# Kernel tuning notes

Measured on AMD Instinct MI355X. Metric: run time of the kernel, lower is better.

## Reference

```python
import jax, jax.numpy as jnp
import numpy as np

NUM_HEADS = 8
LN_EPS = 1e-5


def _layernorm(x, g, b):
    mu = jnp.mean(x, axis=-1, keepdims=True)
    var = jnp.mean((x - mu) ** 2, axis=-1, keepdims=True)
    return (x - mu) * jax.lax.rsqrt(var + LN_EPS) * g + b


def setup_inputs() -> dict:
    key = jax.random.key(0)
    B, T, N, D = 16, 12, 325, 128
    F = 256
    ks = jax.random.split(key, 16)
    s = 0.02
    return {
        "x": jax.random.normal(ks[0], (B, T, N, D), dtype=jnp.float32),
        "Wq": jax.random.normal(ks[1], (D, D), dtype=jnp.float32) * s,
        "bq": jnp.zeros((D,), jnp.float32),
        "Wk": jax.random.normal(ks[2], (D, D), dtype=jnp.float32) * s,
        "bk": jnp.zeros((D,), jnp.float32),
        "Wv": jax.random.normal(ks[3], (D, D), dtype=jnp.float32) * s,
        "bv": jnp.zeros((D,), jnp.float32),
        "Wo": jax.random.normal(ks[4], (D, D), dtype=jnp.float32) * s,
        "bo": jnp.zeros((D,), jnp.float32),
        "ln1_g": jnp.ones((D,), jnp.float32),
        "ln1_b": jnp.zeros((D,), jnp.float32),
        "W1": jax.random.normal(ks[5], (D, F), dtype=jnp.float32) * s,
        "b1": jnp.zeros((F,), jnp.float32),
        "W2": jax.random.normal(ks[6], (F, D), dtype=jnp.float32) * s,
        "b2": jnp.zeros((D,), jnp.float32),
        "ln2_g": jnp.ones((D,), jnp.float32),
        "ln2_b": jnp.zeros((D,), jnp.float32),
    }


def reference(x, Wq, bq, Wk, bk, Wv, bv, Wo, bo, ln1_g, ln1_b, W1, b1, W2, b2, ln2_g, ln2_b):
    B, T, N, D = x.shape
    H = NUM_HEADS
    hd = D // H
    # Conv2d 1x1 projections == per-channel linear over last dim
    q = (x @ Wq + bq).reshape(B, T, N, H, hd)
    k = (x @ Wk + bk).reshape(B, T, N, H, hd)
    v = (x @ Wv + bv).reshape(B, T, N, H, hd)
    # attention across the node dim (n,m), per (batch, head, time)
    scores = jnp.einsum("btnhd,btmhd->bhtnm", q, k) / jnp.sqrt(jnp.float32(hd))
    attn = jax.nn.softmax(scores, axis=-1)
    out = jnp.einsum("bhtnm,btmhd->btnhd", attn, v).reshape(B, T, N, D)
    out = out @ Wo + bo
    out = _layernorm(x + out, ln1_g, ln1_b)
    ffn = jax.nn.gelu(out @ W1 + b1, approximate=False) @ W2 + b2
    return _layernorm(out + ffn, ln2_g, ln2_b)
```

## Files before the change

### kernel.cpp

```cpp
#include <hip/hip_runtime.h>
#include <hip/hip_bf16.h>
#include <math.h>

#define B_ 16
#define T_ 12
#define N_ 325
#define D_ 128
#define H_ 8
#define HD_ 16
#define F_ 256
#define ROWS (B_*T_*N_)
#define NP 336
#define QK_STRIDE 20
#define VT_STRIDE 340
#define LN_EPS 1e-5f

typedef __hip_bfloat16 bf16;
typedef __attribute__((ext_vector_type(8))) short bf16x8;
typedef __attribute__((ext_vector_type(4))) short bf16x4;
typedef __attribute__((ext_vector_type(4))) float f32x4;

__device__ __forceinline__ float b2f(bf16 v) { return __bfloat162float(v); }
__device__ __forceinline__ bf16  f2b(float v) { return __float2bfloat16(v); }

__device__ __forceinline__ float fexp2(float v) { return __builtin_amdgcn_exp2f(v); }
__device__ __forceinline__ float frcp(float v) { return __builtin_amdgcn_rcpf(v); }

union frag_cvt  { uint4 u; bf16x8 s; };
union frag4_cvt { uint2 u; bf16x4 s; };
union h2u       { __hip_bfloat162 h; unsigned u; };

__device__ __forceinline__ bf16x8 frag_ld(const void* p) {
    frag_cvt c; c.u = *(const uint4*)p; return c.s;
}
__device__ __forceinline__ bf16x4 frag4_ld(const void* p) {
    frag4_cvt c; c.u = *(const uint2*)p; return c.s;
}

__device__ __forceinline__ unsigned pk2(float a, float b) {
    h2u c; c.h = __float22bfloat162_rn(make_float2(a, b)); return c.u;
}

__device__ __forceinline__ bf16x4 pack4_rtn(f32x4 v) {
    frag4_cvt c;
    c.u.x = pk2(v[0], v[1]);
    c.u.y = pk2(v[2], v[3]);
    return c.s;
}

__device__ __forceinline__ bf16x8 pack8_rtn(float4 a, float4 b) {
    frag_cvt c;
    c.u.x = pk2(a.x, a.y);
    c.u.y = pk2(a.z, a.w);
    c.u.z = pk2(b.x, b.y);
    c.u.w = pk2(b.z, b.w);
    return c.s;
}

__device__ __forceinline__ float gelu_fast(float a) {
    float z = fexp2(2.3022083f * a * (1.f + 0.044715f * a * a));
    return a * z * frcp(z + 1.f);
}

#define MFMA16(a_, b_, c_) __builtin_amdgcn_mfma_f32_16x16x16bf16_1k((a_), (b_), (c_), 0, 0, 0)
#define MFMA32(a_, b_, c_) __builtin_amdgcn_mfma_f32_16x16x32_bf16((a_), (b_), (c_), 0, 0, 0)

__global__ void convert_weights(const float* __restrict__ Wq, const float* __restrict__ Wk,
                                const float* __restrict__ Wv, const float* __restrict__ Wo,
                                const float* __restrict__ W1, const float* __restrict__ W2,
                                bf16* __restrict__ wt) {
    int i = blockIdx.x * 256 + threadIdx.x;
    if (i < 16384)       { int k = i >> 7, n = i & 127;                    wt[n * 128 + k] = f2b(Wq[i]); }
    else if (i < 32768)  { int j = i - 16384; int k = j >> 7, n = j & 127; wt[16384 + n * 128 + k] = f2b(Wk[j]); }
    else if (i < 49152)  { int j = i - 32768; int k = j >> 7, n = j & 127; wt[32768 + n * 128 + k] = f2b(Wv[j]); }
    else if (i < 65536)  { int j = i - 49152; int k = j >> 7, n = j & 127;
                           wt[49152 + n * 128 + (k ^ ((n & 7) << 3))] = f2b(Wo[j]); }
    else if (i < 98304)  { int j = i - 65536; int k = j >> 8, n = j & 255;
                           wt[65536 + n * 128 + (k ^ ((n & 7) << 3))] = f2b(W1[j]); }
    else                 { int j = i - 98304; int k = j >> 7, n = j & 127;
                           wt[98304 + n * 256 + (k ^ ((n & 7) << 3))] = f2b(W2[j]); }
}

__global__ __launch_bounds__(256) void qkv_attn_kernel(
        const float* __restrict__ x, const bf16* __restrict__ wt,
        const float* __restrict__ bq, const float* __restrict__ bk,
        const float* __restrict__ bv, bf16* __restrict__ ao) {
    __shared__ __align__(16) bf16 qsh[NP * QK_STRIDE];
    __shared__ __align__(16) bf16 ksh[NP * QK_STRIDE];
    __shared__ __align__(16) bf16 vsh_t[HD_ * VT_STRIDE];

    int bid  = blockIdx.x;
    int bt   = bid % 192;
    int h    = bid / 192;
    int tid  = threadIdx.x;
    int wave = tid >> 6;
    int lane = tid & 63;
    int lm   = lane & 15;
    int quad = lane >> 4;

    bf16x8 bfrag[3][4];
    #pragma unroll
    for (int mat = 0; mat < 3; mat++) {
        const bf16* Wt = wt + mat * 16384 + (size_t)(h * 16 + lm) * 128;
        #pragma unroll
        for (int ks = 0; ks < 4; ks++)
            bfrag[mat][ks] = frag_ld(Wt + ks * 32 + quad * 8);
    }
    float bqv = bq[h * 16 + lm], bkv = bk[h * 16 + lm], bvv = bv[h * 16 + lm];
    const float QSCALE = 0.25f * 1.44269504f;

    const float* xslab = x + (size_t)bt * N_ * D_;
    for (int mt = wave; mt < 21; mt += 4) {
        int row  = mt * 16 + lm;
        int crow = row < N_ ? row : N_ - 1;
        const float* xr = xslab + (size_t)crow * D_;
        bf16x8 af[4];
        #pragma unroll
        for (int ks = 0; ks < 4; ks++) {
            const float4* p = (const float4*)(xr + ks * 32 + quad * 8);
            af[ks] = pack8_rtn(p[0], p[1]);
        }
        f32x4 cq = {0.f,0.f,0.f,0.f}, ck = {0.f,0.f,0.f,0.f}, cv = {0.f,0.f,0.f,0.f};
        #pragma unroll
        for (int ks = 0; ks < 4; ks++) {
            cq = MFMA32(af[ks], bfrag[0][ks], cq);
            ck = MFMA32(af[ks], bfrag[1][ks], ck);
            cv = MFMA32(af[ks], bfrag[2][ks], cv);
        }
        #pragma unroll
        for (int reg = 0; reg < 4; reg++) {
            int r = mt * 16 + quad * 4 + reg;
            bool v = r < N_;
            qsh[r * QK_STRIDE + lm]  = f2b(v ? (cq[reg] + bqv) * QSCALE : 0.f);
            ksh[r * QK_STRIDE + lm]  = f2b(v ? (ck[reg] + bkv) : 0.f);
            vsh_t[lm * VT_STRIDE + r] = f2b(v ? (cv[reg] + bvv) : 0.f);
        }
    }
    __syncthreads();

    const f32x4 zero = {0.f, 0.f, 0.f, 0.f};
    for (int qt0 = wave; qt0 < 21; qt0 += 8) {
        int qt1  = qt0 + 4;
        int qt1c = qt1 < 21 ? qt1 : 20;
        bf16x4 qf0 = frag4_ld(qsh + (qt0  * 16 + lm) * QK_STRIDE + quad * 4);
        bf16x4 qf1 = frag4_ld(qsh + (qt1c * 16 + lm) * QK_STRIDE + quad * 4);
        f32x4 o0 = zero, o1 = zero;
        float L0 = 0.f, L1 = 0.f;
        for (int kt = 0; kt < 20; kt++) {
            bf16x4 kf = frag4_ld(ksh + (kt * 16 + lm) * QK_STRIDE + quad * 4);
            bf16x4 vf = frag4_ld(vsh_t + lm * VT_STRIDE + kt * 16 + quad * 4);
            f32x4 s0 = MFMA16(kf, qf0, zero);
            f32x4 s1 = MFMA16(kf, qf1, zero);
            f32x4 p0, p1;
            p0[0] = fexp2(s0[0]); p0[1] = fexp2(s0[1]);
            p0[2] = fexp2(s0[2]); p0[3] = fexp2(s0[3]);
            p1[0] = fexp2(s1[0]); p1[1] = fexp2(s1[1]);
            p1[2] = fexp2(s1[2]); p1[3] = fexp2(s1[3]);
            L0 += (p0[0] + p0[1]) + (p0[2] + p0[3]);
            L1 += (p1[0] + p1[1]) + (p1[2] + p1[3]);
            o0 = MFMA16(vf, pack4_rtn(p0), o0);
            o1 = MFMA16(vf, pack4_rtn(p1), o1);
        }
        {
            bf16x4 kf = frag4_ld(ksh + (20 * 16 + lm) * QK_STRIDE + quad * 4);
            bf16x4 vf = frag4_ld(vsh_t + lm * VT_STRIDE + 20 * 16 + quad * 4);
            f32x4 s0 = MFMA16(kf, qf0, zero);
            f32x4 s1 = MFMA16(kf, qf1, zero);
            f32x4 p0, p1;
            #pragma unroll
            for (int reg = 0; reg < 4; reg++) {
                bool ok = (quad * 4 + reg) < 5;
                p0[reg] = ok ? fexp2(s0[reg]) : 0.f;
                p1[reg] = ok ? fexp2(s1[reg]) : 0.f;
            }
            L0 += (p0[0] + p0[1]) + (p0[2] + p0[3]);
            L1 += (p1[0] + p1[1]) + (p1[2] + p1[3]);
            o0 = MFMA16(vf, pack4_rtn(p0), o0);
            o1 = MFMA16(vf, pack4_rtn(p1), o1);
        }
        L0 += __shfl_xor(L0, 16, 64); L0 += __shfl_xor(L0, 32, 64);
        L1 += __shfl_xor(L1, 16, 64); L1 += __shfl_xor(L1, 32, 64);
        float i0 = frcp(L0), i1 = frcp(L1);
        int n0 = qt0 * 16 + lm;
        if (n0 < N_) {
            frag4_cvt o;
            o.u.x = pk2(o0[0] * i0, o0[1] * i0);
            o.u.y = pk2(o0[2] * i0, o0[3] * i0);
            *(uint2*)(ao + ((size_t)bt * N_ + n0) * D_ + h * HD_ + quad * 4) = o.u;
        }
        int n1 = qt1 * 16 + lm;
        if (qt1 < 21 && n1 < N_) {
            frag4_cvt o;
            o.u.x = pk2(o1[0] * i1, o1[1] * i1);
            o.u.y = pk2(o1[2] * i1, o1[3] * i1);
            *(uint2*)(ao + ((size_t)bt * N_ + n1) * D_ + h * HD_ + quad * 4) = o.u;
        }
    }
}

#define US_STRIDE 136
#define H_STRIDE  264

__global__ __launch_bounds__(256) void epi_a(
        const float* __restrict__ x, const bf16* __restrict__ ao,
        const bf16* __restrict__ wt, const float* __restrict__ bo,
        const float* __restrict__ g1, const float* __restrict__ be1,
        bf16* __restrict__ usg) {
    __shared__ __align__(16) bf16 wbuf[16384];

    const bf16* Wot = wt + 49152;
    int tid  = threadIdx.x;
    int wave = tid >> 6;
    int lm   = tid & 15;
    int quad = (tid & 63) >> 4;
    int r0   = blockIdx.x * 64 + wave * 16;
    int sw   = (lm & 7) << 3;

    bf16x8 afrag[4];
    {
        const bf16* ar = ao + (size_t)(r0 + lm) * D_;
        #pragma unroll
        for (int ks = 0; ks < 4; ks++)
            afrag[ks] = frag_ld(ar + ks * 32 + quad * 8);
    }
    {
        const uint4* gs = (const uint4*)Wot;
        uint4*       ls = (uint4*)wbuf;
        #pragma unroll
        for (int i = 0; i < 8; i++) ls[tid + i * 256] = gs[tid + i * 256];
    }
    __syncthreads();

    f32x4 acc[8];
    #pragma unroll
    for (int nt = 0; nt < 8; nt++) {
        f32x4 c = {0.f, 0.f, 0.f, 0.f};
        const bf16* w = wbuf + (size_t)(nt * 16 + lm) * 128;
        #pragma unroll
        for (int ks = 0; ks < 4; ks++) {
            bf16x8 b = frag_ld(w + ((ks * 32 + quad * 8) ^ sw));
            c = MFMA32(afrag[ks], b, c);
        }
        acc[nt] = c;
    }

    float bov[8], g1v[8], be1v[8];
    #pragma unroll
    for (int nt = 0; nt < 8; nt++) {
        int col = nt * 16 + lm;
        bov[nt] = bo[col]; g1v[nt] = g1[col]; be1v[nt] = be1[col];
    }
    #pragma unroll
    for (int rg = 0; rg < 4; rg++) {
        int grow = r0 + quad * 4 + rg;
        const float* xr = x + (size_t)grow * D_;
        float rr[8];
        float s = 0.f, s2 = 0.f;
        #pragma unroll
        for (int nt = 0; nt < 8; nt++) {
            rr[nt] = acc[nt][rg] + bov[nt] + xr[nt * 16 + lm];
            s += rr[nt]; s2 += rr[nt] * rr[nt];
        }
        #pragma unroll
        for (int mk = 1; mk < 16; mk <<= 1) {
            s += __shfl_xor(s, mk, 64); s2 += __shfl_xor(s2, mk, 64);
        }
        float mu  = s * (1.f / 128.f);
        float var = s2 * (1.f / 128.f) - mu * mu;
        float rstd = rsqrtf(var + LN_EPS);
        bf16* ur = usg + (size_t)grow * D_;
        #pragma unroll
        for (int nt = 0; nt < 8; nt++)
            ur[nt * 16 + lm] = f2b((rr[nt] - mu) * rstd * g1v[nt] + be1v[nt]);
    }
}

__global__ __launch_bounds__(256) void epi_b(
        const bf16* __restrict__ usg, const bf16* __restrict__ wt,
        const float* __restrict__ fb1, const float* __restrict__ fb2,
        const float* __restrict__ g2, const float* __restrict__ be2,
        float* __restrict__ out) {
    __shared__ __align__(16) bf16 wbuf[16384];
    __shared__ __align__(16) bf16 h_lds[4][16 * H_STRIDE];

    const bf16* W1t = wt + 65536;
    const bf16* W2t = wt + 98304;

    int tid  = threadIdx.x;
    int wave = tid >> 6;
    int lm   = tid & 15;
    int quad = (tid & 63) >> 4;
    int r0   = blockIdx.x * 64 + wave * 16;
    int sw   = (lm & 7) << 3;

    bf16* hh = h_lds[wave];
    bf16x8 afrag[8];

    {
        const bf16* ur = usg + (size_t)(r0 + lm) * D_;
        #pragma unroll
        for (int ks = 0; ks < 4; ks++)
            afrag[ks] = frag_ld(ur + ks * 32 + quad * 8);
    }
    {
        const uint4* gs = (const uint4*)W1t;
        uint4*       ls = (uint4*)wbuf;
        #pragma unroll
        for (int i = 0; i < 8; i++) ls[tid + i * 256] = gs[tid + i * 256];
    }
    __syncthreads();

    #pragma unroll
    for (int nt = 0; nt < 8; nt++) {
        f32x4 c = {0.f, 0.f, 0.f, 0.f};
        const bf16* w = wbuf + (size_t)(nt * 16 + lm) * 128;
        #pragma unroll
        for (int ks = 0; ks < 4; ks++) {
            bf16x8 b = frag_ld(w + ((ks * 32 + quad * 8) ^ sw));
            c = MFMA32(afrag[ks], b, c);
        }
        int col = nt * 16 + lm;
        float fb = fb1[col];
        #pragma unroll
        for (int rg = 0; rg < 4; rg++)
            hh[(quad * 4 + rg) * H_STRIDE + col] = f2b(gelu_fast(c[rg] + fb));
    }
    __syncthreads();

    {
        const uint4* gs = ((const uint4*)W1t) + 2048;
        uint4*       ls = (uint4*)wbuf;
        #pragma unroll
        for (int i = 0; i < 8; i++) ls[tid + i * 256] = gs[tid + i * 256];
    }
    __syncthreads();

    #pragma unroll
    for (int nt = 8; nt < 16; nt++) {
        f32x4 c = {0.f, 0.f, 0.f, 0.f};
        const bf16* w = wbuf + (size_t)((nt - 8) * 16 + lm) * 128;
        #pragma unroll
        for (int ks = 0; ks < 4; ks++) {
            bf16x8 b = frag_ld(w + ((ks * 32 + quad * 8) ^ sw));
            c = MFMA32(afrag[ks], b, c);
        }
        int col = nt * 16 + lm;
        float fb = fb1[col];
        #pragma unroll
        for (int rg = 0; rg < 4; rg++)
            hh[(quad * 4 + rg) * H_STRIDE + col] = f2b(gelu_fast(c[rg] + fb));
    }
    __syncthreads();

    #pragma unroll
    for (int ks = 0; ks < 8; ks++)
        afrag[ks] = frag_ld(&hh[lm * H_STRIDE + ks * 32 + quad * 8]);
    {
        const uint4* gs = (const uint4*)W2t;
        uint4*       ls = (uint4*)wbuf;
        #pragma unroll
        for (int i = 0; i < 8; i++) ls[tid + i * 256] = gs[tid + i * 256];
    }
    __syncthreads();

    f32x4 acc[8];
    #pragma unroll
    for (int nt = 0; nt < 4; nt++) {
        f32x4 c = {0.f, 0.f, 0.f, 0.f};
        const bf16* w = wbuf + (size_t)(nt * 16 + lm) * 256;
        #pragma unroll
        for (int ks = 0; ks < 8; ks++) {
            bf16x8 b = frag_ld(w + ((ks * 32 + quad * 8) ^ sw));
            c = MFMA32(afrag[ks], b, c);
        }
        acc[nt] = c;
    }
    __syncthreads();

    {
        const uint4* gs = ((const uint4*)W2t) + 2048;
        uint4*       ls = (uint4*)wbuf;
        #pragma unroll
        for (int i = 0; i < 8; i++) ls[tid + i * 256] = gs[tid + i * 256];
    }
    __syncthreads();

    #pragma unroll
    for (int nt = 4; nt < 8; nt++) {
        f32x4 c = {0.f, 0.f, 0.f, 0.f};
        const bf16* w = wbuf + (size_t)((nt - 4) * 16 + lm) * 256;
        #pragma unroll
        for (int ks = 0; ks < 8; ks++) {
            bf16x8 b = frag_ld(w + ((ks * 32 + quad * 8) ^ sw));
            c = MFMA32(afrag[ks], b, c);
        }
        acc[nt] = c;
    }
    float fb2v[8], g2v[8], be2v[8];
    #pragma unroll
    for (int nt = 0; nt < 8; nt++) {
        int col = nt * 16 + lm;
        fb2v[nt] = fb2[col]; g2v[nt] = g2[col]; be2v[nt] = be2[col];
    }
    #pragma unroll
    for (int rg = 0; rg < 4; rg++) {
        int grow = r0 + quad * 4 + rg;
        const bf16* ur = usg + (size_t)grow * D_;
        float yy[8];
        float s = 0.f, s2 = 0.f;
        #pragma unroll
        for (int nt = 0; nt < 8; nt++) {
            yy[nt] = acc[nt][rg] + fb2v[nt] + b2f(ur[nt * 16 + lm]);
            s += yy[nt]; s2 += yy[nt] * yy[nt];
        }
        #pragma unroll
        for (int mk = 1; mk < 16; mk <<= 1) {
            s += __shfl_xor(s, mk, 64); s2 += __shfl_xor(s2, mk, 64);
        }
        float mu  = s * (1.f / 128.f);
        float var = s2 * (1.f / 128.f) - mu * mu;
        float rstd = rsqrtf(var + LN_EPS);
        float* orow = out + (size_t)grow * D_;
        #pragma unroll
        for (int nt = 0; nt < 8; nt++)
            orow[nt * 16 + lm] = (yy[nt] - mu) * rstd * g2v[nt] + be2v[nt];
    }
}

__global__ __launch_bounds__(256) void epilogue_mfma(
        const float* __restrict__ x, const bf16* __restrict__ ao,
        const bf16* __restrict__ wt,
        const float* __restrict__ bo,
        const float* __restrict__ g1, const float* __restrict__ be1,
        const float* __restrict__ fb1, const float* __restrict__ fb2,
        const float* __restrict__ g2, const float* __restrict__ be2,
        float* __restrict__ out) {
    __shared__ __align__(16) bf16 bufA[16384];
    __shared__ __align__(16) bf16 bufB[16384];
    __shared__ __align__(16) bf16 bufC[16384];
    __shared__ __align__(16) bf16 us_lds[4][16 * US_STRIDE];
    __shared__ __align__(16) bf16 h_lds[4][16 * H_STRIDE];

    const bf16* Wot = wt + 49152;
    const bf16* W1t = wt + 65536;
    const bf16* W2t = wt + 98304;

    int tid  = threadIdx.x;
    int wave = tid >> 6;
    int lm   = tid & 15;
    int quad = (tid & 63) >> 4;
    int r0   = blockIdx.x * 64 + wave * 16;
    int sw   = (lm & 7) << 3;

    bf16* us = us_lds[wave];
    bf16* hh = h_lds[wave];

    bf16x8 afrag[8];
    {
        const bf16* ar = ao + (size_t)(r0 + lm) * D_;
        #pragma unroll
        for (int ks = 0; ks < 4; ks++)
            afrag[ks] = frag_ld(ar + ks * 32 + quad * 8);
    }
    {
        const uint4* gs0 = (const uint4*)Wot;
        const uint4* gs1 = (const uint4*)W1t;
        uint4* lA = (uint4*)bufA;
        uint4* lB = (uint4*)bufB;
        #pragma unroll
        for (int i = 0; i < 8; i++) lA[tid + i * 256] = gs0[tid + i * 256];
        #pragma unroll
        for (int i = 0; i < 8; i++) lB[tid + i * 256] = gs1[tid + i * 256];
    }
    __syncthreads();

    f32x4 acc[8];
    #pragma unroll
    for (int nt = 0; nt < 8; nt++) {
        f32x4 c = {0.f, 0.f, 0.f, 0.f};
        const bf16* w = bufA + (size_t)(nt * 16 + lm) * 128;
        #pragma unroll
        for (int ks = 0; ks < 4; ks++) {
            bf16x8 b = frag_ld(w + ((ks * 32 + quad * 8) ^ sw));
            c = MFMA32(afrag[ks], b, c);
        }
        acc[nt] = c;
    }
    float bov[8], g1v[8], be1v[8], g2v[8], be2v[8], fb2v[8];
    #pragma unroll
    for (int nt = 0; nt < 8; nt++) {
        int col = nt * 16 + lm;
        bov[nt] = bo[col]; g1v[nt] = g1[col]; be1v[nt] = be1[col];
        g2v[nt] = g2[col]; be2v[nt] = be2[col]; fb2v[nt] = fb2[col];
    }
    float usv[8][4];
    #pragma unroll
    for (int rg = 0; rg < 4; rg++) {
        int grow = r0 + quad * 4 + rg;
        const float* xr = x + (size_t)grow * D_;
        float rr[8];
        float s = 0.f, s2 = 0.f;
        #pragma unroll
        for (int nt = 0; nt < 8; nt++) {
            rr[nt] = acc[nt][rg] + bov[nt] + xr[nt * 16 + lm];
            s += rr[nt]; s2 += rr[nt] * rr[nt];
        }
        #pragma unroll
        for (int mk = 1; mk < 16; mk <<= 1) {
            s += __shfl_xor(s, mk, 64); s2 += __shfl_xor(s2, mk, 64);
        }
        float mu  = s * (1.f / 128.f);
        float var = s2 * (1.f / 128.f) - mu * mu;
        float rstd = rsqrtf(var + LN_EPS);
        int lrow = quad * 4 + rg;
        #pragma unroll
        for (int nt = 0; nt < 8; nt++) {
            float u = (rr[nt] - mu) * rstd * g1v[nt] + be1v[nt];
            usv[nt][rg] = u;
            us[lrow * US_STRIDE + nt * 16 + lm] = f2b(u);
        }
    }
    {
        const uint4* gs = ((const uint4*)W1t) + 2048;
        uint4* lC = (uint4*)bufC;
        #pragma unroll
        for (int i = 0; i < 8; i++) lC[tid + i * 256] = gs[tid + i * 256];
    }
    __syncthreads();

    #pragma unroll
    for (int ks = 0; ks < 4; ks++)
        afrag[ks] = frag_ld(&us[lm * US_STRIDE + ks * 32 + quad * 8]);
    #pragma unroll
    for (int nt = 0; nt < 8; nt++) {
        f32x4 c = {0.f, 0.f, 0.f, 0.f};
        const bf16* w = bufB + (size_t)(nt * 16 + lm) * 128;
        #pragma unroll
        for (int ks = 0; ks < 4; ks++) {
            bf16x8 b = frag_ld(w + ((ks * 32 + quad * 8) ^ sw));
            c = MFMA32(afrag[ks], b, c);
        }
        int col = nt * 16 + lm;
        float fb = fb1[col];
        #pragma unroll
        for (int rg = 0; rg < 4; rg++)
            hh[(quad * 4 + rg) * H_STRIDE + col] = f2b(gelu_fast(c[rg] + fb));
    }
    #pragma unroll
    for (int nt = 8; nt < 16; nt++) {
        f32x4 c = {0.f, 0.f, 0.f, 0.f};
        const bf16* w = bufC + (size_t)((nt - 8) * 16 + lm) * 128;
        #pragma unroll
        for (int ks = 0; ks < 4; ks++) {
            bf16x8 b = frag_ld(w + ((ks * 32 + quad * 8) ^ sw));
            c = MFMA32(afrag[ks], b, c);
        }
        int col = nt * 16 + lm;
        float fb = fb1[col];
        #pragma unroll
        for (int rg = 0; rg < 4; rg++)
            hh[(quad * 4 + rg) * H_STRIDE + col] = f2b(gelu_fast(c[rg] + fb));
    }
    {
        const uint4* gs = (const uint4*)W2t;
        uint4* lA = (uint4*)bufA;
        #pragma unroll
        for (int i = 0; i < 8; i++) lA[tid + i * 256] = gs[tid + i * 256];
    }
    __syncthreads();

    #pragma unroll
    for (int ks = 0; ks < 8; ks++)
        afrag[ks] = frag_ld(&hh[lm * H_STRIDE + ks * 32 + quad * 8]);
    #pragma unroll
    for (int nt = 0; nt < 4; nt++) {
        f32x4 c = {0.f, 0.f, 0.f, 0.f};
        const bf16* w = bufA + (size_t)(nt * 16 + lm) * 256;
        #pragma unroll
        for (int ks = 0; ks < 8; ks++) {
            bf16x8 b = frag_ld(w + ((ks * 32 + quad * 8) ^ sw));
            c = MFMA32(afrag[ks], b, c);
        }
        acc[nt] = c;
    }
    {
        const uint4* gs = ((const uint4*)W2t) + 2048;
        uint4* lB = (uint4*)bufB;
        #pragma unroll
        for (int i = 0; i < 8; i++) lB[tid + i * 256] = gs[tid + i * 256];
    }
    __syncthreads();

    #pragma unroll
    for (int nt = 4; nt < 8; nt++) {
        f32x4 c = {0.f, 0.f, 0.f, 0.f};
        const bf16* w = bufB + (size_t)((nt - 4) * 16 + lm) * 256;
        #pragma unroll
        for (int ks = 0; ks < 8; ks++) {
            bf16x8 b = frag_ld(w + ((ks * 32 + quad * 8) ^ sw));
            c = MFMA32(afrag[ks], b, c);
        }
        acc[nt] = c;
    }
    #pragma unroll
    for (int rg = 0; rg < 4; rg++) {
        float yy[8];
        float s = 0.f, s2 = 0.f;
        #pragma unroll
        for (int nt = 0; nt < 8; nt++) {
            yy[nt] = acc[nt][rg] + fb2v[nt] + usv[nt][rg];
            s += yy[nt]; s2 += yy[nt] * yy[nt];
        }
        #pragma unroll
        for (int mk = 1; mk < 16; mk <<= 1) {
            s += __shfl_xor(s, mk, 64); s2 += __shfl_xor(s2, mk, 64);
        }
        float mu  = s * (1.f / 128.f);
        float var = s2 * (1.f / 128.f) - mu * mu;
        float rstd = rsqrtf(var + LN_EPS);
        int grow = r0 + quad * 4 + rg;
        float* orow = out + (size_t)grow * D_;
        #pragma unroll
        for (int nt = 0; nt < 8; nt++)
            orow[nt * 16 + lm] = (yy[nt] - mu) * rstd * g2v[nt] + be2v[nt];
    }
}

extern "C" void kernel_launch(void* const* d_in, const int* in_sizes, int n_in,
                              void* d_out, int out_size, void* d_ws, size_t ws_size,
                              hipStream_t stream) {
    const float* x   = (const float*)d_in[0];
    const float* Wq  = (const float*)d_in[1];
    const float* bq  = (const float*)d_in[2];
    const float* Wk  = (const float*)d_in[3];
    const float* bk  = (const float*)d_in[4];
    const float* Wv  = (const float*)d_in[5];
    const float* bv  = (const float*)d_in[6];
    const float* Wo  = (const float*)d_in[7];
    const float* bo  = (const float*)d_in[8];
    const float* g1  = (const float*)d_in[9];
    const float* be1 = (const float*)d_in[10];
    const float* W1  = (const float*)d_in[11];
    const float* fb1 = (const float*)d_in[12];
    const float* W2  = (const float*)d_in[13];
    const float* fb2 = (const float*)d_in[14];
    const float* g2  = (const float*)d_in[15];
    const float* be2 = (const float*)d_in[16];
    float* out = (float*)d_out;

    bf16* wt  = (bf16*)d_ws;
    bf16* ao  = wt + 131072;
    bf16* usg = ao + (size_t)ROWS * D_;
    const size_t need_split = (size_t)(131072 + 2 * (size_t)ROWS * D_) * sizeof(bf16);
    bool split = ws_size >= need_split;

    convert_weights<<<512, 256, 0, stream>>>(Wq, Wk, Wv, Wo, W1, W2, wt);
    qkv_attn_kernel<<<B_ * T_ * H_, 256, 0, stream>>>(x, wt, bq, bk, bv, ao);
    if (split) {
        epi_a<<<ROWS / 64, 256, 0, stream>>>(x, ao, wt, bo, g1, be1, usg);
        epi_b<<<ROWS / 64, 256, 0, stream>>>(usg, wt, fb1, fb2, g2, be2, out);
    } else {
        epilogue_mfma<<<ROWS / 64, 256, 0, stream>>>(x, ao, wt, bo, g1, be1, fb1,
                                                     fb2, g2, be2, out);
    }
}
```

Measured before the change: 202.8 us.

## Split FFN epilogue into separate W1+GELU and W2+LayerNorm kernels

Splits the fused FFN kernel into two launches: one computes GELU(u·W1+b1) and writes the bf16 hidden activations to a global buffer, the other reads them back for W2, the residual and the second LayerNorm. Each kernel uses less LDS and fewer registers, which may raise occupancy. In exchange the ROWS×256 bf16 hidden tensor, roughly 32 MB, is written and then re-read through HBM, plus one extra launch. The new path runs only when the workspace is large enough.

```diff
diff --git a/kernel.cpp b/kernel.cpp
--- a/kernel.cpp
+++ b/kernel.cpp
@@ -275,6 +275,170 @@
     }
 }
 
+__global__ __launch_bounds__(256) void epi_b1(
+        const bf16* __restrict__ usg, const bf16* __restrict__ wt,
+        const float* __restrict__ fb1, bf16* __restrict__ hg) {
+    __shared__ __align__(16) bf16 wbuf[16384];
+
+    const bf16* W1t = wt + 65536;
+    int tid  = threadIdx.x;
+    int wave = tid >> 6;
+    int lm   = tid & 15;
+    int quad = (tid & 63) >> 4;
+    int r0   = blockIdx.x * 64 + wave * 16;
+    int sw   = (lm & 7) << 3;
+
+    bf16x8 afrag[4];
+    {
+        const bf16* ur = usg + (size_t)(r0 + lm) * D_;
+        #pragma unroll
+        for (int ks = 0; ks < 4; ks++)
+            afrag[ks] = frag_ld(ur + ks * 32 + quad * 8);
+    }
+    {
+        const uint4* gs = (const uint4*)W1t;
+        uint4*       ls = (uint4*)wbuf;
+        #pragma unroll
+        for (int i = 0; i < 8; i++) ls[tid + i * 256] = gs[tid + i * 256];
+    }
+    __syncthreads();
+
+    #pragma unroll
+    for (int nt = 0; nt < 8; nt++) {
+        f32x4 c = {0.f, 0.f, 0.f, 0.f};
+        const bf16* w = wbuf + (size_t)(nt * 16 + lm) * 128;
+        #pragma unroll
+        for (int ks = 0; ks < 4; ks++) {
+            bf16x8 b = frag_ld(w + ((ks * 32 + quad * 8) ^ sw));
+            c = MFMA32(afrag[ks], b, c);
+        }
+        int col = nt * 16 + lm;
+        float fb = fb1[col];
+        #pragma unroll
+        for (int rg = 0; rg < 4; rg++)
+            hg[(size_t)(r0 + quad * 4 + rg) * F_ + col] = f2b(gelu_fast(c[rg] + fb));
+    }
+    __syncthreads();
+
+    {
+        const uint4* gs = ((const uint4*)W1t) + 2048;
+        uint4*       ls = (uint4*)wbuf;
+        #pragma unroll
+        for (int i = 0; i < 8; i++) ls[tid + i * 256] = gs[tid + i * 256];
+    }
+    __syncthreads();
+
+    #pragma unroll
+    for (int nt = 8; nt < 16; nt++) {
+        f32x4 c = {0.f, 0.f, 0.f, 0.f};
+        const bf16* w = wbuf + (size_t)((nt - 8) * 16 + lm) * 128;
+        #pragma unroll
+        for (int ks = 0; ks < 4; ks++) {
+            bf16x8 b = frag_ld(w + ((ks * 32 + quad * 8) ^ sw));
+            c = MFMA32(afrag[ks], b, c);
+        }
+        int col = nt * 16 + lm;
+        float fb = fb1[col];
+        #pragma unroll
+        for (int rg = 0; rg < 4; rg++)
+            hg[(size_t)(r0 + quad * 4 + rg) * F_ + col] = f2b(gelu_fast(c[rg] + fb));
+    }
+}
+
+__global__ __launch_bounds__(256) void epi_b2(
+        const bf16* __restrict__ usg, const bf16* __restrict__ hg,
+        const bf16* __restrict__ wt,
+        const float* __restrict__ fb2, const float* __restrict__ g2,
+        const float* __restrict__ be2, float* __restrict__ out) {
+    __shared__ __align__(16) bf16 wbuf[16384];
+
+    const bf16* W2t = wt + 98304;
+    int tid  = threadIdx.x;
+    int wave = tid >> 6;
+    int lm   = tid & 15;
+    int quad = (tid & 63) >> 4;
+    int r0   = blockIdx.x * 64 + wave * 16;
+    int sw   = (lm & 7) << 3;
+
+    bf16x8 afrag[8];
+    {
+        const bf16* hr = hg + (size_t)(r0 + lm) * F_;
+        #pragma unroll
+        for (int ks = 0; ks < 8; ks++)
+            afrag[ks] = frag_ld(hr + ks * 32 + quad * 8);
+    }
+    {
+        const uint4* gs = (const uint4*)W2t;
+        uint4*       ls = (uint4*)wbuf;
+        #pragma unroll
+        for (int i = 0; i < 8; i++) ls[tid + i * 256] = gs[tid + i * 256];
+    }
+    __syncthreads();
+
+    f32x4 acc[8];
+    #pragma unroll
+    for (int nt = 0; nt < 4; nt++) {
+        f32x4 c = {0.f, 0.f, 0.f, 0.f};
+        const bf16* w = wbuf + (size_t)(nt * 16 + lm) * 256;
+        #pragma unroll
+        for (int ks = 0; ks < 8; ks++) {
+            bf16x8 b = frag_ld(w + ((ks * 32 + quad * 8) ^ sw));
+            c = MFMA32(afrag[ks], b, c);
+        }
+        acc[nt] = c;
+    }
+    __syncthreads();
+
+    {
+        const uint4* gs = ((const uint4*)W2t) + 2048;
+        uint4*       ls = (uint4*)wbuf;
+        #pragma unroll
+        for (int i = 0; i < 8; i++) ls[tid + i * 256] = gs[tid + i * 256];
+    }
+    __syncthreads();
+
+    #pragma unroll
+    for (int nt = 4; nt < 8; nt++) {
+        f32x4 c = {0.f, 0.f, 0.f, 0.f};
+        const bf16* w = wbuf + (size_t)((nt - 4) * 16 + lm) * 256;
+        #pragma unroll
+        for (int ks = 0; ks < 8; ks++) {
+            bf16x8 b = frag_ld(w + ((ks * 32 + quad * 8) ^ sw));
+            c = MFMA32(afrag[ks], b, c);
+        }
+        acc[nt] = c;
+    }
+    float fb2v[8], g2v[8], be2v[8];
+    #pragma unroll
+    for (int nt = 0; nt < 8; nt++) {
+        int col = nt * 16 + lm;
+        fb2v[nt] = fb2[col]; g2v[nt] = g2[col]; be2v[nt] = be2[col];
+    }
+    #pragma unroll
+    for (int rg = 0; rg < 4; rg++) {
+        int grow = r0 + quad * 4 + rg;
+        const bf16* ur = usg + (size_t)grow * D_;
+        float yy[8];
+        float s = 0.f, s2 = 0.f;
+        #pragma unroll
+        for (int nt = 0; nt < 8; nt++) {
+            yy[nt] = acc[nt][rg] + fb2v[nt] + b2f(ur[nt * 16 + lm]);
+            s += yy[nt]; s2 += yy[nt] * yy[nt];
+        }
+        #pragma unroll
+        for (int mk = 1; mk < 16; mk <<= 1) {
+            s += __shfl_xor(s, mk, 64); s2 += __shfl_xor(s2, mk, 64);
+        }
+        float mu  = s * (1.f / 128.f);
+        float var = s2 * (1.f / 128.f) - mu * mu;
+        float rstd = rsqrtf(var + LN_EPS);
+        float* orow = out + (size_t)grow * D_;
+        #pragma unroll
+        for (int nt = 0; nt < 8; nt++)
+            orow[nt * 16 + lm] = (yy[nt] - mu) * rstd * g2v[nt] + be2v[nt];
+    }
+}
+
 __global__ __launch_bounds__(256) void epi_b(
         const bf16* __restrict__ usg, const bf16* __restrict__ wt,
         const float* __restrict__ fb1, const float* __restrict__ fb2,
@@ -651,12 +815,19 @@
     bf16* wt  = (bf16*)d_ws;
     bf16* ao  = wt + 131072;
     bf16* usg = ao + (size_t)ROWS * D_;
-    const size_t need_split = (size_t)(131072 + 2 * (size_t)ROWS * D_) * sizeof(bf16);
-    bool split = ws_size >= need_split;
+    bf16* hg  = usg + (size_t)ROWS * D_;
+    const size_t need1 = (size_t)(131072 + 2 * (size_t)ROWS * D_) * sizeof(bf16);
+    const size_t need2 = need1 + (size_t)ROWS * F_ * sizeof(bf16);
+    bool split2 = ws_size >= need2;
+    bool split1 = ws_size >= need1;
 
     convert_weights<<<512, 256, 0, stream>>>(Wq, Wk, Wv, Wo, W1, W2, wt);
     qkv_attn_kernel<<<B_ * T_ * H_, 256, 0, stream>>>(x, wt, bq, bk, bv, ao);
-    if (split) {
+    if (split2) {
+        epi_a<<<ROWS / 64, 256, 0, stream>>>(x, ao, wt, bo, g1, be1, usg);
+        epi_b1<<<ROWS / 64, 256, 0, stream>>>(usg, wt, fb1, hg);
+        epi_b2<<<ROWS / 64, 256, 0, stream>>>(usg, hg, wt, fb2, g2, be2, out);
+    } else if (split1) {
         epi_a<<<ROWS / 64, 256, 0, stream>>>(x, ao, wt, bo, g1, be1, usg);
         epi_b<<<ROWS / 64, 256, 0, stream>>>(usg, wt, fb1, fb2, g2, be2, out);
     } else {
```

Result: slower. 213.5 us (+5.3%).
